# Performance work log

Hardware: AMD Instinct MI355X
Metric: run time of the kernel (lower is better)

The kernel has to match this reference:

```python
import jax, jax.numpy as jnp
import numpy as np

N_NODES = 100000
N_EDGES = 600000
HIDDEN = 128


def setup_inputs() -> dict:
    key = jax.random.key(0)
    ks = jax.random.split(key, 5)
    x = jax.random.normal(ks[0], (N_NODES, HIDDEN), dtype=jnp.float32)
    edge_index = jax.random.randint(ks[1], (2, N_EDGES), 0, N_NODES, dtype=jnp.int64)
    edge_weight = jax.random.uniform(ks[2], (N_EDGES,), dtype=jnp.float32)
    # MLP params: Linear(2*H+1 -> H), ReLU, Linear(H -> 1)
    W1 = jax.random.normal(ks[3], (2 * HIDDEN + 1, HIDDEN), dtype=jnp.float32) * (1.0 / np.sqrt(2 * HIDDEN + 1))
    b1 = jnp.zeros((HIDDEN,), dtype=jnp.float32)
    W2 = jax.random.normal(ks[4], (HIDDEN, 1), dtype=jnp.float32) * (1.0 / np.sqrt(HIDDEN))
    b2 = jnp.zeros((1,), dtype=jnp.float32)
    return {"x": x, "edge_index": edge_index, "edge_weight": edge_weight,
            "W1": W1, "b1": b1, "W2": W2, "b2": b2}


def reference(x, edge_index, edge_weight, W1, b1, W2, b2):
    num_nodes = x.shape[0]
    src = edge_index[0]
    tgt = edge_index[1]
    h_src = x[src]                      # [E, H] gather
    h_tgt = x[tgt]                      # [E, H] gather
    w = edge_weight[:, None]            # [E, 1]
    concat = jnp.concatenate([h_src, h_tgt, w], axis=-1)   # [E, 2H+1]
    hidden = jax.nn.relu(concat @ W1 + b1)                 # [E, H]
    scores = (hidden @ W2 + b2)[:, 0]                      # [E]
    # NOTE: the original _softmax_edge's max-pass uses index_put_(accumulate=True)
    # on a -inf buffer, so every touched entry stays -inf and is then replaced by 0;
    # the net effect is NO max subtraction. Faithful math: plain exp / segment_sum.
    exp_scores = jnp.exp(scores)
    sum_exp = jax.ops.segment_sum(exp_scores, tgt, num_segments=num_nodes)
    sum_exp = jnp.maximum(sum_exp, 1e-12)
    alpha = exp_scores / sum_exp[tgt]                      # [E]
    out = jax.ops.segment_sum(alpha[:, None] * h_src, tgt, num_segments=num_nodes)
    return x + out
```

## Files before the change

### kernel.cpp

```cpp
#include <hip/hip_runtime.h>
#include <hip/hip_bf16.h>

#define N_NODES 100000
#define N_EDGES 600000
#define HID 128
#define SCAN_NB ((N_NODES + 255) / 256)


typedef short bf16x8 __attribute__((ext_vector_type(8)));
typedef float f32x4  __attribute__((ext_vector_type(4)));

__device__ inline unsigned short f2bf(float v) {
    __hip_bfloat16 h = __float2bfloat16(v);
    return *(unsigned short*)&h;
}
__device__ inline float bf2f(unsigned short s) {
    unsigned int u = (unsigned int)s << 16;
    return __uint_as_float(u);
}
__device__ inline float2 bfpair(unsigned int u) {
    float lo = __uint_as_float(u << 16);
    float hi = __uint_as_float(u & 0xffff0000u);
    return make_float2(lo, hi);
}

__global__ __launch_bounds__(256) void k_prep(const float* __restrict__ W1,
                                              unsigned short* __restrict__ Bh,
                                              int* __restrict__ deg)
{
    int idx = blockIdx.x * 256 + threadIdx.x;
    if (idx < N_NODES) deg[idx] = 0;
    if (idx < 32768) {
        int n = idx & 255;
        int k = idx >> 8;
        float v = (n < HID) ? W1[k * HID + n] : W1[(HID + k) * HID + (n - HID)];
        int dst = (k >> 5) * 8192 + n * 32 + (k & 31);
        Bh[dst] = f2bf(v);
    }
}

__global__ __launch_bounds__(256) void k_gemm(const float* __restrict__ x,
                                              const unsigned short* __restrict__ BhG,
                                              unsigned short* __restrict__ zbuf,
                                              unsigned short* __restrict__ y2buf)
{
    __shared__ unsigned short Ah[64 * 32];

    const int tid  = threadIdx.x;
    const int bm   = blockIdx.x * 64;
    const int wave = tid >> 6;
    const int lane = tid & 63;
    const int q    = lane >> 4;
    const int ln   = lane & 15;

    const int rowA = tid >> 3;
    const int rowB = rowA + 32;
    const int f4   = tid & 7;
    const int gmA  = bm + rowA;
    const int gmB  = bm + rowB;
    const bool okA = gmA < N_NODES;
    const bool okB = gmB < N_NODES;
    const float* pxA = &x[(size_t)gmA * HID + f4 * 4];
    const float* pxB = &x[(size_t)gmB * HID + f4 * 4];

    f32x4 acc[4][4] = {};

    float4 vA = make_float4(0.f,0.f,0.f,0.f), vB = vA;
    float4 vAn = vA, vBn = vA;
    if (okA) vA = *(const float4*)pxA;
    if (okB) vB = *(const float4*)pxB;

    for (int ks = 0; ks < 4; ++ks) {
        const int k0 = ks * 32;
        {
            float4 v = vA;
            unsigned int ph0 = (unsigned int)f2bf(v.x) | ((unsigned int)f2bf(v.y) << 16);
            unsigned int ph1 = (unsigned int)f2bf(v.z) | ((unsigned int)f2bf(v.w) << 16);
            *(uint2*)&Ah[rowA * 32 + f4 * 4] = make_uint2(ph0, ph1);
            if (okA) *(uint2*)&zbuf[(size_t)gmA * 256 + 128 + k0 + f4 * 4] = make_uint2(ph0, ph1);
        }
        {
            float4 v = vB;
            unsigned int ph0 = (unsigned int)f2bf(v.x) | ((unsigned int)f2bf(v.y) << 16);
            unsigned int ph1 = (unsigned int)f2bf(v.z) | ((unsigned int)f2bf(v.w) << 16);
            *(uint2*)&Ah[rowB * 32 + f4 * 4] = make_uint2(ph0, ph1);
            if (okB) *(uint2*)&zbuf[(size_t)gmB * 256 + 128 + k0 + f4 * 4] = make_uint2(ph0, ph1);
        }
        __syncthreads();

        if (ks < 3) {
            vAn = okA ? *(const float4*)(pxA + (ks + 1) * 32) : make_float4(0.f,0.f,0.f,0.f);
            vBn = okB ? *(const float4*)(pxB + (ks + 1) * 32) : make_float4(0.f,0.f,0.f,0.f);
        }

        bf16x8 ah[4], bh[4];
        #pragma unroll
        for (int mt = 0; mt < 4; ++mt) {
            ah[mt] = *(const bf16x8*)&Ah[(mt * 16 + ln) * 32 + q * 8];
        }
        #pragma unroll
        for (int nt = 0; nt < 4; ++nt) {
            bh[nt] = *(const bf16x8*)&BhG[ks * 8192 + (wave * 64 + nt * 16 + ln) * 32 + q * 8];
        }
        #pragma unroll
        for (int mt = 0; mt < 4; ++mt) {
            #pragma unroll
            for (int nt = 0; nt < 4; ++nt) {
                acc[mt][nt] = __builtin_amdgcn_mfma_f32_16x16x32_bf16(ah[mt], bh[nt], acc[mt][nt], 0, 0, 0);
            }
        }
        __syncthreads();
        vA = vAn; vB = vBn;
    }

    #pragma unroll
    for (int mt = 0; mt < 4; ++mt) {
        #pragma unroll
        for (int r = 0; r < 4; ++r) {
            int row = bm + mt * 16 + q * 4 + r;
            if (row < N_NODES) {
                #pragma unroll
                for (int nt = 0; nt < 4; ++nt) {
                    int col = wave * 64 + nt * 16 + ln;
                    unsigned short v = f2bf(acc[mt][nt][r]);
                    if (col < 128) zbuf[(size_t)row * 256 + col] = v;
                    else           y2buf[(size_t)row * 128 + (col - 128)] = v;
                }
            }
        }
    }
}

__global__ __launch_bounds__(256) void k_count(const int* __restrict__ ei,
                                               int* __restrict__ deg)
{
    int e = blockIdx.x * blockDim.x + threadIdx.x;
    if (e < N_EDGES) atomicAdd(&deg[ei[N_EDGES + e]], 1);
}

__global__ __launch_bounds__(256) void k_partial(const int* __restrict__ deg,
                                                 int* __restrict__ partial)
{
    __shared__ int s[256];
    int t = threadIdx.x;
    int idx = blockIdx.x * 256 + t;
    s[t] = (idx < N_NODES) ? deg[idx] : 0;
    __syncthreads();
    #pragma unroll
    for (int off = 128; off > 0; off >>= 1) {
        if (t < off) s[t] += s[t + off];
        __syncthreads();
    }
    if (t == 0) partial[blockIdx.x] = s[0];
}

__global__ __launch_bounds__(512) void k_scanp(const int* __restrict__ partial,
                                               int* __restrict__ pbase)
{
    __shared__ int s[512];
    int t = threadIdx.x;
    int v = (t < SCAN_NB) ? partial[t] : 0;
    s[t] = v;
    __syncthreads();
    #pragma unroll
    for (int off = 1; off < 512; off <<= 1) {
        int u = (t >= off) ? s[t - off] : 0;
        __syncthreads();
        s[t] += u;
        __syncthreads();
    }
    if (t < SCAN_NB) pbase[t] = s[t] - v;
}

__global__ __launch_bounds__(256) void k_rowptr(const int* __restrict__ deg,
                                                const int* __restrict__ pbase,
                                                int* __restrict__ rowptr,
                                                int* __restrict__ cursor)
{
    __shared__ int s[256];
    int t = threadIdx.x;
    int b = blockIdx.x;
    int idx = b * 256 + t;
    int v = (idx < N_NODES) ? deg[idx] : 0;
    s[t] = v;
    __syncthreads();
    #pragma unroll
    for (int off = 1; off < 256; off <<= 1) {
        int u = (t >= off) ? s[t - off] : 0;
        __syncthreads();
        s[t] += u;
        __syncthreads();
    }
    if (idx < N_NODES) {
        int r = pbase[b] + s[t] - v;
        rowptr[idx] = r;
        cursor[idx] = r;
    }
    if (idx == 0) rowptr[N_NODES] = N_EDGES;
}

__global__ __launch_bounds__(256) void k_fill(const int* __restrict__ ei,
                                              const float* __restrict__ ew,
                                              int* __restrict__ cursor,
                                              uint2* __restrict__ eprs)
{
    int e = blockIdx.x * blockDim.x + threadIdx.x;
    if (e >= N_EDGES) return;
    int tgt = ei[N_EDGES + e];
    int pos = atomicAdd(&cursor[tgt], 1);
    eprs[pos] = make_uint2((unsigned int)ei[e], __float_as_uint(ew[e]));
}

__global__ __launch_bounds__(256) void k_fused(const unsigned int* __restrict__ zu,
                                               const unsigned int* __restrict__ y2u,
                                               const int* __restrict__ rowptr,
                                               const uint2* __restrict__ eprs,
                                               const float* __restrict__ x,
                                               const float* __restrict__ W1,
                                               const float* __restrict__ b1,
                                               const float* __restrict__ W2,
                                               const float* __restrict__ b2,
                                               float* __restrict__ out)
{
    int n = (blockIdx.x * blockDim.x + threadIdx.x) >> 6;
    int lane = threadIdx.x & 63;
    if (n >= N_NODES) return;
    int ql = lane & 15;
    int qi = lane >> 4;
    int c0 = ql * 8;

    uint4 uy2 = *(const uint4*)&y2u[(size_t)n * 64 + ql * 4];
    float2 y2a = bfpair(uy2.x), y2b = bfpair(uy2.y), y2c = bfpair(uy2.z), y2d = bfpair(uy2.w);
    float4 bv0 = *(const float4*)&b1[c0];
    float4 bv1 = *(const float4*)&b1[c0 + 4];
    float4 wr0 = *(const float4*)&W1[256 * HID + c0];
    float4 wr1 = *(const float4*)&W1[256 * HID + c0 + 4];
    float4 w20 = *(const float4*)&W2[c0];
    float4 w21 = *(const float4*)&W2[c0 + 4];
    float p0 = y2a.x + bv0.x, p1 = y2a.y + bv0.y, p2 = y2b.x + bv0.z, p3 = y2b.y + bv0.w;
    float p4 = y2c.x + bv1.x, p5 = y2c.y + bv1.y, p6 = y2d.x + bv1.z, p7 = y2d.y + bv1.w;
    float b2v = b2[0];

    int beg = rowptr[n], end = rowptr[n + 1];
    float a0 = 0.f, a1 = 0.f, a2 = 0.f, a3 = 0.f;
    float a4 = 0.f, a5 = 0.f, a6 = 0.f, a7 = 0.f;
    float denom = 0.f;

    for (int i = beg; i < end; i += 4) {
        int idx = i + qi;
        bool valid = idx < end;
        int ie = valid ? idx : (end - 1);
        uint2 ep = eprs[ie];
        size_t base = (size_t)ep.x * 128;
        float w = __uint_as_float(ep.y);
        uint4 uy = *(const uint4*)&zu[base + ql * 4];
        uint4 ux = *(const uint4*)&zu[base + 64 + ql * 4];

        float2 ya = bfpair(uy.x), yb = bfpair(uy.y), yc = bfpair(uy.z), yd = bfpair(uy.w);
        float h0 = fmaxf(fmaf(w, wr0.x, ya.x + p0), 0.f);
        float h1 = fmaxf(fmaf(w, wr0.y, ya.y + p1), 0.f);
        float h2 = fmaxf(fmaf(w, wr0.z, yb.x + p2), 0.f);
        float h3 = fmaxf(fmaf(w, wr0.w, yb.y + p3), 0.f);
        float h4 = fmaxf(fmaf(w, wr1.x, yc.x + p4), 0.f);
        float h5 = fmaxf(fmaf(w, wr1.y, yc.y + p5), 0.f);
        float h6 = fmaxf(fmaf(w, wr1.z, yd.x + p6), 0.f);
        float h7 = fmaxf(fmaf(w, wr1.w, yd.y + p7), 0.f);
        float s = ((h0 * w20.x + h1 * w20.y) + (h2 * w20.z + h3 * w20.w))
                + ((h4 * w21.x + h5 * w21.y) + (h6 * w21.z + h7 * w21.w));
        #pragma unroll
        for (int m = 1; m <= 8; m <<= 1) s += __shfl_xor(s, m, 64);
        float es = valid ? __expf(s + b2v) : 0.f;

        float2 xa = bfpair(ux.x), xb = bfpair(ux.y), xc = bfpair(ux.z), xd = bfpair(ux.w);
        a0 = fmaf(es, xa.x, a0); a1 = fmaf(es, xa.y, a1);
        a2 = fmaf(es, xb.x, a2); a3 = fmaf(es, xb.y, a3);
        a4 = fmaf(es, xc.x, a4); a5 = fmaf(es, xc.y, a5);
        a6 = fmaf(es, xd.x, a6); a7 = fmaf(es, xd.y, a7);
        denom += es;
    }

    #pragma unroll
    for (int m = 16; m <= 32; m <<= 1) {
        a0 += __shfl_xor(a0, m, 64); a1 += __shfl_xor(a1, m, 64);
        a2 += __shfl_xor(a2, m, 64); a3 += __shfl_xor(a3, m, 64);
        a4 += __shfl_xor(a4, m, 64); a5 += __shfl_xor(a5, m, 64);
        a6 += __shfl_xor(a6, m, 64); a7 += __shfl_xor(a7, m, 64);
        denom += __shfl_xor(denom, m, 64);
    }

    if (qi == 0) {
        float4 xt0 = *(const float4*)&x[(size_t)n * HID + c0];
        float4 xt1 = *(const float4*)&x[(size_t)n * HID + c0 + 4];
        float inv = 1.0f / fmaxf(denom, 1e-12f);
        float4 o0, o1;
        o0.x = xt0.x + a0 * inv; o0.y = xt0.y + a1 * inv;
        o0.z = xt0.z + a2 * inv; o0.w = xt0.w + a3 * inv;
        o1.x = xt1.x + a4 * inv; o1.y = xt1.y + a5 * inv;
        o1.z = xt1.z + a6 * inv; o1.w = xt1.w + a7 * inv;
        *(float4*)&out[(size_t)n * HID + c0]     = o0;
        *(float4*)&out[(size_t)n * HID + c0 + 4] = o1;
    }
}

extern "C" void kernel_launch(void* const* d_in, const int* in_sizes, int n_in,
                              void* d_out, int out_size, void* d_ws, size_t ws_size,
                              hipStream_t stream) {
    const float* x  = (const float*)d_in[0];
    const int*   ei = (const int*)d_in[1];
    const float* ew = (const float*)d_in[2];
    const float* W1 = (const float*)d_in[3];
    const float* b1 = (const float*)d_in[4];
    const float* W2 = (const float*)d_in[5];
    const float* b2 = (const float*)d_in[6];
    float* out = (float*)d_out;
    char* ws = (char*)d_ws;

    const size_t deg_b    = 400000;
    const size_t rowptr_b = 400016;
    const size_t cursor_b = 400000;
    const size_t eprs_b   = 4800000;
    const size_t part_b   = 1568;
    const size_t pb_b     = 1568;
    const size_t Bh_b     = 65536;

    char* p = ws;
    int* deg      = (int*)p;             p += deg_b;
    int* rowptr   = (int*)p;             p += rowptr_b;
    int* cursor   = (int*)p;             p += cursor_b;
    uint2* eprs   = (uint2*)p;           p += eprs_b;
    int* partial  = (int*)p;             p += part_b;
    int* pbase    = (int*)p;             p += pb_b;
    unsigned short* BhG = (unsigned short*)p;  p += Bh_b;
    unsigned short* zbuf  = (unsigned short*)p;  p += (size_t)N_NODES * 256 * 2;
    unsigned short* y2buf = (unsigned short*)p;

    const int edge_blocks = (N_EDGES + 255) / 256;
    const int node_wave_blocks = (N_NODES * 64 + 255) / 256;
    const int gemm_blocks = (N_NODES + 63) / 64;

    hipLaunchKernelGGL(k_prep, dim3(SCAN_NB), dim3(256), 0, stream, W1, BhG, deg);
    hipLaunchKernelGGL(k_count, dim3(edge_blocks), dim3(256), 0, stream, ei, deg);
    hipLaunchKernelGGL(k_partial, dim3(SCAN_NB), dim3(256), 0, stream, deg, partial);
    hipLaunchKernelGGL(k_scanp, dim3(1), dim3(512), 0, stream, partial, pbase);
    hipLaunchKernelGGL(k_rowptr, dim3(SCAN_NB), dim3(256), 0, stream, deg, pbase, rowptr, cursor);
    hipLaunchKernelGGL(k_fill, dim3(edge_blocks), dim3(256), 0, stream, ei, ew, cursor, eprs);
    hipLaunchKernelGGL(k_gemm, dim3(gemm_blocks), dim3(256), 0, stream, x, BhG, zbuf, y2buf);
    hipLaunchKernelGGL(k_fused, dim3(node_wave_blocks), dim3(256), 0, stream,
                       (const unsigned int*)zbuf, (const unsigned int*)y2buf,
                       rowptr, eprs, x, W1, b1, W2, b2, out);
}
```

Before: 279.5 us.

## Merge CSR construction kernels into one cooperative kernel with grid syncs

Replaces the six separate launches (prep, count, partial sums, scan, rowptr, fill) with a single cooperative persistent kernel of 1280 blocks that separates the phases with grid.sync(). The aim is to remove per-launch overhead and the gaps between small dependent kernels. In exchange it adds grid-wide barriers and requires every block to be co-resident. Throughput on the atomic-heavy phases may drop because the grid is fixed in size.

```diff
diff --git a/kernel.cpp b/kernel.cpp
--- a/kernel.cpp
+++ b/kernel.cpp
@@ -1,10 +1,14 @@
 #include <hip/hip_runtime.h>
 #include <hip/hip_bf16.h>
+#include <hip/hip_cooperative_groups.h>
+
+namespace cg = cooperative_groups;
 
 #define N_NODES 100000
 #define N_EDGES 600000
 #define HID 128
 #define SCAN_NB ((N_NODES + 255) / 256)
+#define CSR_BLOCKS 1280
 
 
 typedef short bf16x8 __attribute__((ext_vector_type(8)));
@@ -24,18 +28,95 @@
     return make_float2(lo, hi);
 }
 
-__global__ __launch_bounds__(256) void k_prep(const float* __restrict__ W1,
-                                              unsigned short* __restrict__ Bh,
-                                              int* __restrict__ deg)
+__global__ __launch_bounds__(256, 8) void k_csr(const int* __restrict__ ei,
+                                                const float* __restrict__ ew,
+                                                const float* __restrict__ W1,
+                                                int* __restrict__ deg,
+                                                int* __restrict__ rowptr,
+                                                int* __restrict__ cursor,
+                                                int* __restrict__ partial,
+                                                int* __restrict__ pbase,
+                                                unsigned short* __restrict__ Bh,
+                                                uint2* __restrict__ eprs)
 {
-    int idx = blockIdx.x * 256 + threadIdx.x;
-    if (idx < N_NODES) deg[idx] = 0;
-    if (idx < 32768) {
-        int n = idx & 255;
-        int k = idx >> 8;
+    cg::grid_group grid = cg::this_grid();
+    __shared__ int sm[1024];
+    const int t   = threadIdx.x;
+    const int b   = blockIdx.x;
+    const int gid = b * 256 + t;
+    const int gsz = CSR_BLOCKS * 256;
+
+    for (int i = gid; i < N_NODES; i += gsz) deg[i] = 0;
+    for (int i = gid; i < 32768; i += gsz) {
+        int n = i & 255;
+        int k = i >> 8;
         float v = (n < HID) ? W1[k * HID + n] : W1[(HID + k) * HID + (n - HID)];
-        int dst = (k >> 5) * 8192 + n * 32 + (k & 31);
-        Bh[dst] = f2bf(v);
+        Bh[(k >> 5) * 8192 + n * 32 + (k & 31)] = f2bf(v);
+    }
+    grid.sync();
+
+    for (int e = gid; e < N_EDGES; e += gsz) {
+        atomicAdd(&deg[ei[N_EDGES + e]], 1);
+    }
+    grid.sync();
+
+    if (b < SCAN_NB) {
+        int idx = b * 256 + t;
+        sm[t] = (idx < N_NODES) ? deg[idx] : 0;
+        __syncthreads();
+        #pragma unroll
+        for (int off = 128; off > 0; off >>= 1) {
+            if (t < off) sm[t] += sm[t + off];
+            __syncthreads();
+        }
+        if (t == 0) partial[b] = sm[0];
+    }
+    grid.sync();
+
+    if (b == 0) {
+        int o0 = (t < SCAN_NB) ? partial[t] : 0;
+        int o1 = (t + 256 < SCAN_NB) ? partial[t + 256] : 0;
+        sm[t] = o0;
+        sm[t + 256] = o1;
+        __syncthreads();
+        for (int off = 1; off < 512; off <<= 1) {
+            int v0 = sm[t]       + ((t >= off)       ? sm[t - off]       : 0);
+            int v1 = sm[t + 256] + ((t + 256 >= off) ? sm[t + 256 - off] : 0);
+            __syncthreads();
+            sm[t] = v0;
+            sm[t + 256] = v1;
+            __syncthreads();
+        }
+        if (t < SCAN_NB) pbase[t] = sm[t] - o0;
+        if (t + 256 < SCAN_NB) pbase[t + 256] = sm[t + 256] - o1;
+    }
+    grid.sync();
+
+    if (b < SCAN_NB) {
+        int idx = b * 256 + t;
+        int v = (idx < N_NODES) ? deg[idx] : 0;
+        sm[t] = v;
+        __syncthreads();
+        #pragma unroll
+        for (int off = 1; off < 256; off <<= 1) {
+            int u = (t >= off) ? sm[t - off] : 0;
+            __syncthreads();
+            sm[t] += u;
+            __syncthreads();
+        }
+        if (idx < N_NODES) {
+            int r = pbase[b] + sm[t] - v;
+            rowptr[idx] = r;
+            cursor[idx] = r;
+        }
+        if (idx == 0) rowptr[N_NODES] = N_EDGES;
+    }
+    grid.sync();
+
+    for (int e = gid; e < N_EDGES; e += gsz) {
+        int tgt = ei[N_EDGES + e];
+        int pos = atomicAdd(&cursor[tgt], 1);
+        eprs[pos] = make_uint2((unsigned int)ei[e], __float_as_uint(ew[e]));
     }
 }
 
@@ -129,86 +210,6 @@
             }
         }
     }
-}
-
-__global__ __launch_bounds__(256) void k_count(const int* __restrict__ ei,
-                                               int* __restrict__ deg)
-{
-    int e = blockIdx.x * blockDim.x + threadIdx.x;
-    if (e < N_EDGES) atomicAdd(&deg[ei[N_EDGES + e]], 1);
-}
-
-__global__ __launch_bounds__(256) void k_partial(const int* __restrict__ deg,
-                                                 int* __restrict__ partial)
-{
-    __shared__ int s[256];
-    int t = threadIdx.x;
-    int idx = blockIdx.x * 256 + t;
-    s[t] = (idx < N_NODES) ? deg[idx] : 0;
-    __syncthreads();
-    #pragma unroll
-    for (int off = 128; off > 0; off >>= 1) {
-        if (t < off) s[t] += s[t + off];
-        __syncthreads();
-    }
-    if (t == 0) partial[blockIdx.x] = s[0];
-}
-
-__global__ __launch_bounds__(512) void k_scanp(const int* __restrict__ partial,
-                                               int* __restrict__ pbase)
-{
-    __shared__ int s[512];
-    int t = threadIdx.x;
-    int v = (t < SCAN_NB) ? partial[t] : 0;
-    s[t] = v;
-    __syncthreads();
-    #pragma unroll
-    for (int off = 1; off < 512; off <<= 1) {
-        int u = (t >= off) ? s[t - off] : 0;
-        __syncthreads();
-        s[t] += u;
-        __syncthreads();
-    }
-    if (t < SCAN_NB) pbase[t] = s[t] - v;
-}
-
-__global__ __launch_bounds__(256) void k_rowptr(const int* __restrict__ deg,
-                                                const int* __restrict__ pbase,
-                                                int* __restrict__ rowptr,
-                                                int* __restrict__ cursor)
-{
-    __shared__ int s[256];
-    int t = threadIdx.x;
-    int b = blockIdx.x;
-    int idx = b * 256 + t;
-    int v = (idx < N_NODES) ? deg[idx] : 0;
-    s[t] = v;
-    __syncthreads();
-    #pragma unroll
-    for (int off = 1; off < 256; off <<= 1) {
-        int u = (t >= off) ? s[t - off] : 0;
-        __syncthreads();
-        s[t] += u;
-        __syncthreads();
-    }
-    if (idx < N_NODES) {
-        int r = pbase[b] + s[t] - v;
-        rowptr[idx] = r;
-        cursor[idx] = r;
-    }
-    if (idx == 0) rowptr[N_NODES] = N_EDGES;
-}
-
-__global__ __launch_bounds__(256) void k_fill(const int* __restrict__ ei,
-                                              const float* __restrict__ ew,
-                                              int* __restrict__ cursor,
-                                              uint2* __restrict__ eprs)
-{
-    int e = blockIdx.x * blockDim.x + threadIdx.x;
-    if (e >= N_EDGES) return;
-    int tgt = ei[N_EDGES + e];
-    int pos = atomicAdd(&cursor[tgt], 1);
-    eprs[pos] = make_uint2((unsigned int)ei[e], __float_as_uint(ew[e]));
 }
 
 __global__ __launch_bounds__(256) void k_fused(const unsigned int* __restrict__ zu,
@@ -334,16 +335,16 @@
     unsigned short* zbuf  = (unsigned short*)p;  p += (size_t)N_NODES * 256 * 2;
     unsigned short* y2buf = (unsigned short*)p;
 
-    const int edge_blocks = (N_EDGES + 255) / 256;
     const int node_wave_blocks = (N_NODES * 64 + 255) / 256;
     const int gemm_blocks = (N_NODES + 63) / 64;
 
-    hipLaunchKernelGGL(k_prep, dim3(SCAN_NB), dim3(256), 0, stream, W1, BhG, deg);
-    hipLaunchKernelGGL(k_count, dim3(edge_blocks), dim3(256), 0, stream, ei, deg);
-    hipLaunchKernelGGL(k_partial, dim3(SCAN_NB), dim3(256), 0, stream, deg, partial);
-    hipLaunchKernelGGL(k_scanp, dim3(1), dim3(512), 0, stream, partial, pbase);
-    hipLaunchKernelGGL(k_rowptr, dim3(SCAN_NB), dim3(256), 0, stream, deg, pbase, rowptr, cursor);
-    hipLaunchKernelGGL(k_fill, dim3(edge_blocks), dim3(256), 0, stream, ei, ew, cursor, eprs);
+    {
+        void* args[] = { (void*)&ei, (void*)&ew, (void*)&W1, (void*)&deg,
+                         (void*)&rowptr, (void*)&cursor, (void*)&partial,
+                         (void*)&pbase, (void*)&BhG, (void*)&eprs };
+        hipLaunchCooperativeKernel((const void*)k_csr, dim3(CSR_BLOCKS), dim3(256),
+                                   args, 0, stream);
+    }
     hipLaunchKernelGGL(k_gemm, dim3(gemm_blocks), dim3(256), 0, stream, x, BhG, zbuf, y2buf);
     hipLaunchKernelGGL(k_fused, dim3(node_wave_blocks), dim3(256), 0, stream,
                        (const unsigned int*)zbuf, (const unsigned int*)y2buf,
```

Measured after the change: 886.9 us. 217% more time.
